# Kernel optimization log

Measured on AMD Instinct MI355X. Metric: run time of the kernel, lower is better.

The kernel has to match this reference:

```python
import jax, jax.numpy as jnp
import numpy as np

B = 1
E = 8388608                      # embedding size (dim 1)
NNZ = 131072                     # inhibition links
MIN_SPARSITY = 0.002
MAX_SPARSITY = 0.02
BOOST_PERCENT = 1e-8             # forward default boost_percent
MAX_ACTIVE = int(np.ceil(MAX_SPARSITY * E))    # 167773, torch uses .item() -> static
MIN_ACTIVE = int(np.floor(MIN_SPARSITY * E))   # 16777


def setup_inputs() -> dict:
    key = jax.random.key(0)
    k1, k3, k4, k5 = jax.random.split(key, 4)
    x = jax.random.normal(k1, (B, E, 1, 1), dtype=jnp.float32)
    boost_tensor = jnp.zeros((B, E, 1, 1), dtype=jnp.float32)   # initial boost state (zeros_like in module)
    inh_affector = jax.random.randint(k3, (NNZ,), 0, E, dtype=jnp.int32)
    inh_affectee = jax.random.randint(k4, (NNZ,), 0, E, dtype=jnp.int32)
    # inhibition values are negative (self-inhibition, affect_value=-0.01 scale)
    inh_values = -jax.random.uniform(k5, (NNZ,), dtype=jnp.float32) * 0.05
    return {"x": x, "boost_tensor": boost_tensor, "inh_values": inh_values,
            "inh_affector": inh_affector, "inh_affectee": inh_affectee}


def reference(x, boost_tensor, inh_values, inh_affector, inh_affectee):
    xf = x.reshape(B, E)
    bf = boost_tensor.reshape(B, E)

    # --- run_boosting: PercentClosenessBoosting (units far from max get boosted) ---
    boost_new = bf + (1.0 - xf / jnp.max(xf)) * jnp.float32(BOOST_PERCENT)
    boosted = jnp.maximum(xf, 0.0) + boost_new   # tensor_above + boost_tensor

    # --- apply_sparse_self_affector: tens[affectee] += tens[affector] * values ---
    # RHS gathered from the pre-update tensor, scatter-add onto affectee coords.
    inhibited = boosted.at[0, inh_affectee].add(boosted[0, inh_affector] * inh_values)

    # --- run_k_winners_positive: keep top max_active per row, binarize positives ---
    topv, topi = jax.lax.top_k(inhibited, MAX_ACTIVE)          # [B, K]
    rows = jnp.arange(B)[:, None]
    result = jnp.zeros((B, E), dtype=jnp.float32).at[rows, topi].set(
        (topv > 0).astype(jnp.float32))

    # --- choose_boosted_to_satisfy_minimum ---
    actually_active = jnp.sum(result)
    _, boost_idx = jax.lax.top_k(boost_new, MIN_ACTIVE)        # [B, MIN_ACTIVE]
    to_activate = jnp.ceil(jnp.float32(MIN_ACTIVE) - actually_active)
    need = actually_active < jnp.float32(MIN_ACTIVE)
    add = need & (jnp.arange(MIN_ACTIVE, dtype=jnp.float32) < to_activate)
    add = jnp.broadcast_to(add.astype(jnp.float32), (B, MIN_ACTIVE))
    out = result.at[rows, boost_idx].max(add)

    return out.reshape(B, E, 1, 1)
```

## Files before the change

kernel.cpp:

```cpp
#include <hip/hip_runtime.h>
#include <stdint.h>

#define E_SIZE   8388608
#define N4       (E_SIZE / 4)
#define NNZ_SZ   131072
#define K_ACT    167773
#define MIN_ACT  16777
#define CAP      262144
#define BCAP     2048
#define TINY_F   9.5367431640625e-7f
#define NBINS    16384
#define SHIFT1   18

__device__ __forceinline__ unsigned int f2A(float f) {
    unsigned int u = __float_as_uint(f);
    return (u & 0x80000000u) ? ~u : (u | 0x80000000u);
}
__device__ __forceinline__ unsigned int f2D(float f) { return ~f2A(f); }
__device__ __forceinline__ float A2f(unsigned int A) {
    unsigned int u = (A & 0x80000000u) ? (A & 0x7FFFFFFFu) : ~A;
    return __uint_as_float(u);
}
__device__ __forceinline__ float D2f(unsigned int D) { return A2f(~D); }

__device__ __forceinline__ float boostedf(float v, float b, float mx) {
    return fmaxf(v, 0.0f) + (b + (1.0f - v / mx) * 1e-8f);
}
__device__ __forceinline__ unsigned int binclamp14(float v) {
    return (v < TINY_F) ? (NBINS - 1u) : (f2D(v) >> SHIFT1);
}


__device__ void block_select(const unsigned int* counts, int nbins, unsigned int Krem,
                             unsigned int* res, unsigned int* scratch) {
    int t = threadIdx.x;
    int per = nbins >> 10; if (per == 0) per = 1;
    int nth = nbins / per;
    unsigned int part = 0;
    if (t < nth)
        for (int j = 0; j < per; j++) part += counts[t * per + j];
    scratch[t] = part;
    unsigned int ws = part;
    for (int off = 32; off; off >>= 1) ws += __shfl_down(ws, off, 64);
    if ((t & 63) == 0) scratch[1024 + (t >> 6)] = ws;
    __syncthreads();
    if (t == 0) {
        unsigned int cum = 0;
        int w = 0;
        for (; w < 15; w++) {
            unsigned int s = scratch[1024 + w];
            if (cum + s >= Krem) break;
            cum += s;
        }
        int tt = w * 64, te = tt + 63;
        for (; tt < te; tt++) {
            unsigned int s = scratch[tt];
            if (cum + s >= Krem) break;
            cum += s;
        }
        int b = tt * per, be = b + per - 1;
        for (; b < be; b++) {
            unsigned int s = counts[b];
            if (cum + s >= Krem) break;
            cum += s;
        }
        res[0] = (unsigned int)b;
        res[1] = Krem - cum;
    }
    __syncthreads();
}

__global__ void __launch_bounds__(256)
k_max(const float4* __restrict__ x, unsigned int* __restrict__ pmax,
      unsigned int* __restrict__ ctrl, unsigned int* __restrict__ hist) {
    int t = threadIdx.x, blk = blockIdx.x;
    if (blk == 0 && t < 64) ctrl[t] = 0u;
    if (t < 16) hist[blk * 16 + t] = 0u;
    int tid = blk * 256 + t;
    unsigned int m = 0u;
    for (int i = tid; i < N4; i += 1024 * 256) {
        float4 v = x[i];
        m = max(m, f2A(v.x)); m = max(m, f2A(v.y));
        m = max(m, f2A(v.z)); m = max(m, f2A(v.w));
    }
    for (int off = 32; off; off >>= 1)
        m = max(m, __shfl_down(m, off, 64));
    __shared__ unsigned int sm[4];
    if ((t & 63) == 0) sm[t >> 6] = m;
    __syncthreads();
    if (t == 0) pmax[blk] = max(max(sm[0], sm[1]), max(sm[2], sm[3]));
}

__device__ __forceinline__ float reduce_pmax(const unsigned int* __restrict__ pmax,
                                             unsigned int* smax) {
    int t = threadIdx.x;
    unsigned int m = pmax[t];
    for (int off = 32; off; off >>= 1)
        m = max(m, __shfl_down(m, off, 64));
    if ((t & 63) == 0) smax[t >> 6] = m;
    __syncthreads();
    if (t == 0) {
        unsigned int r = smax[0];
        for (int i = 1; i < 16; i++) r = max(r, smax[i]);
        smax[0] = r;
    }
    __syncthreads();
    return A2f(smax[0]);
}

__global__ void __launch_bounds__(1024)
k_boost_hist(const float4* __restrict__ x, const float4* __restrict__ bf,
             float4* __restrict__ out, const unsigned int* __restrict__ pmax,
             unsigned int* __restrict__ hist) {
    __shared__ unsigned int h[NBINS];
    __shared__ unsigned int smax[16];
    float mx = reduce_pmax(pmax, smax);
    int t = threadIdx.x;
    for (int i = t; i < NBINS; i += 1024) h[i] = 0u;
    __syncthreads();
    unsigned int tiny = 0;
    int gtid = blockIdx.x * 1024 + t;
    for (int i = gtid; i < N4; i += 512 * 1024) {
        float4 v = x[i], b = bf[i];
        float4 r;
        r.x = boostedf(v.x, b.x, mx);
        r.y = boostedf(v.y, b.y, mx);
        r.z = boostedf(v.z, b.z, mx);
        r.w = boostedf(v.w, b.w, mx);
        out[i] = r;
        #define HISTONE(c) { if ((c) < TINY_F) tiny++; \
            else atomicAdd(&h[f2D(c) >> SHIFT1], 1u); }
        HISTONE(r.x); HISTONE(r.y); HISTONE(r.z); HISTONE(r.w);
        #undef HISTONE
    }
    for (int off = 32; off; off >>= 1)
        tiny += __shfl_down(tiny, off, 64);
    if ((t & 63) == 0 && tiny) atomicAdd(&h[NBINS - 1], tiny);
    __syncthreads();
    for (int k = t; k < NBINS; k += 1024) {
        unsigned int c = h[k];
        if (c) atomicAdd(&hist[k], c);
    }
}

__global__ void __launch_bounds__(1024)
k_scatter(const float* __restrict__ x, const float* __restrict__ bf,
          const float* __restrict__ vals, const int* __restrict__ aff,
          const int* __restrict__ afe, float* __restrict__ inh,
          const unsigned int* __restrict__ pmax, unsigned int* __restrict__ hist) {
    __shared__ int shi[NBINS];
    __shared__ unsigned int smax[16];
    float mx = reduce_pmax(pmax, smax);
    int t = threadIdx.x;
    for (int i = t; i < NBINS; i += 1024) shi[i] = 0;
    __syncthreads();
    int i = blockIdx.x * 1024 + t;
    int a = aff[i], e = afe[i];
    float bo = boostedf(x[a], bf[a], mx);
    float contrib = bo * vals[i];
    float old = atomicAdd(&inh[e], contrib);
    float nw = old + contrib;
    unsigned int ob = binclamp14(old), nb = binclamp14(nw);
    if (ob != nb) {
        atomicAdd(&shi[nb], 1);
        atomicAdd(&shi[ob], -1);
    }
    __syncthreads();
    for (int k = t; k < NBINS; k += 1024) {
        int v = shi[k];
        if (v) atomicAdd((int*)&hist[k], v);
    }
}

__global__ void __launch_bounds__(1024)
k_markselect(float4* __restrict__ out, const unsigned int* __restrict__ hist,
             unsigned int* __restrict__ ctrl, unsigned int* __restrict__ gidx,
             unsigned int* __restrict__ gD) {
    __shared__ unsigned int scratch[1040];
    __shared__ unsigned int res[2];
    __shared__ unsigned int cidx[BCAP];
    __shared__ unsigned int cDs[BCAP];
    __shared__ unsigned int scnt, sbase;
    int t = threadIdx.x;
    if (t == 0) scnt = 0;
    block_select(hist, NBINS, (unsigned int)K_ACT, res, scratch);
    unsigned int b1 = res[0];
    if (blockIdx.x == 0 && t == 0) { ctrl[1] = res[0]; ctrl[2] = res[1]; }
    __syncthreads();
    int gtid = blockIdx.x * 1024 + t;
    for (int i = gtid; i < N4; i += 512 * 1024) {
        float4 f = out[i];
        float4 r;
        #define MARKONE(c, rr, comp) { \
            unsigned int bc = binclamp14(c); \
            if (bc < b1) rr = ((c) > 0.0f) ? 1.0f : 0.0f; \
            else { rr = 0.0f; if (bc == b1) { \
                unsigned int p = atomicAdd(&scnt, 1u); \
                if (p < BCAP) { cidx[p] = (unsigned int)i * 4u + comp; cDs[p] = f2D(c); } } } }
        MARKONE(f.x, r.x, 0u); MARKONE(f.y, r.y, 1u);
        MARKONE(f.z, r.z, 2u); MARKONE(f.w, r.w, 3u);
        #undef MARKONE
        out[i] = r;
    }
    __syncthreads();
    if (t == 0) {
        unsigned int m = min(scnt, (unsigned int)BCAP);
        scnt = m;
        sbase = atomicAdd(&ctrl[7], m);
    }
    __syncthreads();
    unsigned int m = scnt, base = sbase;
    for (unsigned int i = t; i < m; i += 1024) {
        unsigned int g = base + i;
        if (g < CAP) { gidx[g] = cidx[i]; gD[g] = cDs[i]; }
    }
}

__global__ void __launch_bounds__(1024)
k_select(float* __restrict__ out, const unsigned int* __restrict__ ctrl,
         const unsigned int* __restrict__ gidx, const unsigned int* __restrict__ gD) {
    __shared__ unsigned int h512[512];
    __shared__ unsigned int scratch[1040];
    __shared__ unsigned int res[2];
    __shared__ unsigned int ties[128];
    __shared__ unsigned int tcnt;
    int t = threadIdx.x;
    unsigned int nc = min(ctrl[7], (unsigned int)CAP);
    unsigned int Krem = ctrl[2];
    unsigned int b1 = ctrl[1];

    if (t < 512) h512[t] = 0u;
    if (t == 0) tcnt = 0u;
    __syncthreads();
    for (unsigned int i = t; i < nc; i += 1024)
        atomicAdd(&h512[(gD[i] >> 9) & 511u], 1u);
    __syncthreads();
    block_select(h512, 512, Krem, res, scratch);
    unsigned int b2 = res[0], Krem2 = res[1];

    if (t < 512) h512[t] = 0u;
    __syncthreads();
    for (unsigned int i = t; i < nc; i += 1024) {
        unsigned int D = gD[i];
        if (((D >> 9) & 511u) == b2) atomicAdd(&h512[D & 511u], 1u);
    }
    __syncthreads();
    block_select(h512, 512, Krem2, res, scratch);
    unsigned int b3 = res[0], need = res[1];
    unsigned int T = (b1 << SHIFT1) | (b2 << 9) | b3;

    for (unsigned int i = t; i < nc; i += 1024) {
        if (gD[i] == T) {
            unsigned int p = atomicAdd(&tcnt, 1u);
            if (p < 128) ties[p] = gidx[i];
        }
    }
    __syncthreads();
    unsigned int M = min(tcnt, 128u);
    float val = (D2f(T) > 0.0f) ? 1.0f : 0.0f;
    for (unsigned int i = t; i < M; i += 1024) {
        unsigned int idx = ties[i];
        unsigned int rank = 0;
        for (unsigned int j = 0; j < M; j++) rank += (ties[j] < idx) ? 1u : 0u;
        if (rank < need) out[idx] = val;
    }
    for (unsigned int i = t; i < nc; i += 1024) {
        unsigned int D = gD[i];
        if (D < T) out[gidx[i]] = (D2f(D) > 0.0f) ? 1.0f : 0.0f;
    }
}

extern "C" void kernel_launch(void* const* d_in, const int* in_sizes, int n_in,
                              void* d_out, int out_size, void* d_ws, size_t ws_size,
                              hipStream_t stream) {
    const float* x    = (const float*)d_in[0];
    const float* bf   = (const float*)d_in[1];
    const float* vals = (const float*)d_in[2];
    const int*   aff  = (const int*)d_in[3];
    const int*   afe  = (const int*)d_in[4];
    float* out = (float*)d_out;

    unsigned int* ctrl = (unsigned int*)d_ws;
    unsigned int* pmax = (unsigned int*)((char*)d_ws + 4096);
    unsigned int* hist = (unsigned int*)((char*)d_ws + 16384);
    unsigned int* gidx = (unsigned int*)((char*)d_ws + 16384 + (size_t)NBINS * 4);
    unsigned int* gD   = (unsigned int*)((char*)d_ws + 16384 + (size_t)NBINS * 4 + (size_t)CAP * 4);

    k_max<<<1024, 256, 0, stream>>>((const float4*)x, pmax, ctrl, hist);
    k_boost_hist<<<512, 1024, 0, stream>>>((const float4*)x, (const float4*)bf,
                                           (float4*)out, pmax, hist);
    k_scatter<<<NNZ_SZ / 1024, 1024, 0, stream>>>(x, bf, vals, aff, afe, out, pmax, hist);
    k_markselect<<<512, 1024, 0, stream>>>((float4*)out, hist, ctrl, gidx, gD);
    k_select<<<1, 1024, 0, stream>>>(out, ctrl, gidx, gD);
}
```

Before: 190.4 us.

## Fuse max, boost-histogram, scatter and selection into two kernels with grid barriers

```diff
diff --git a/kernel.cpp b/kernel.cpp
--- a/kernel.cpp
+++ b/kernel.cpp
@@ -11,6 +11,11 @@
 #define TINY_F   9.5367431640625e-7f
 #define NBINS    16384
 #define SHIFT1   18
+#define G1       256
+#define G2       512
+
+#define AL(p)  __hip_atomic_load((p), __ATOMIC_RELAXED, __HIP_MEMORY_SCOPE_AGENT)
+#define ALA(p) __hip_atomic_load((p), __ATOMIC_ACQUIRE, __HIP_MEMORY_SCOPE_AGENT)
 
 __device__ __forceinline__ unsigned int f2A(float f) {
     unsigned int u = __float_as_uint(f);
@@ -30,6 +35,14 @@
     return (v < TINY_F) ? (NBINS - 1u) : (f2D(v) >> SHIFT1);
 }
 
+
+__device__ __forceinline__ void grid_spin_barrier(unsigned int* ctr, unsigned int n) {
+    if (threadIdx.x == 0) {
+        __hip_atomic_fetch_add(ctr, 1u, __ATOMIC_ACQ_REL, __HIP_MEMORY_SCOPE_AGENT);
+        while (ALA(ctr) < n) __builtin_amdgcn_s_sleep(1);
+    }
+    __syncthreads();
+}
 
 __device__ void block_select(const unsigned int* counts, int nbins, unsigned int Krem,
                              unsigned int* res, unsigned int* scratch) {
@@ -70,178 +83,207 @@
     __syncthreads();
 }
 
-__global__ void __launch_bounds__(256)
-k_max(const float4* __restrict__ x, unsigned int* __restrict__ pmax,
-      unsigned int* __restrict__ ctrl, unsigned int* __restrict__ hist) {
+__device__ void block_select_g(unsigned int* counts, int nbins, unsigned int Krem,
+                               unsigned int* res, unsigned int* scratch) {
+    int t = threadIdx.x;
+    int per = nbins >> 10;
+    unsigned int part = 0;
+    for (int j = 0; j < per; j++) part += AL(&counts[t * per + j]);
+    scratch[t] = part;
+    unsigned int ws = part;
+    for (int off = 32; off; off >>= 1) ws += __shfl_down(ws, off, 64);
+    if ((t & 63) == 0) scratch[1024 + (t >> 6)] = ws;
+    __syncthreads();
+    if (t == 0) {
+        unsigned int cum = 0;
+        int w = 0;
+        for (; w < 15; w++) {
+            unsigned int s = scratch[1024 + w];
+            if (cum + s >= Krem) break;
+            cum += s;
+        }
+        int tt = w * 64, te = tt + 63;
+        for (; tt < te; tt++) {
+            unsigned int s = scratch[tt];
+            if (cum + s >= Krem) break;
+            cum += s;
+        }
+        int b = tt * per, be = b + per - 1;
+        for (; b < be; b++) {
+            unsigned int s = AL(&counts[b]);
+            if (cum + s >= Krem) break;
+            cum += s;
+        }
+        res[0] = (unsigned int)b;
+        res[1] = Krem - cum;
+    }
+    __syncthreads();
+}
+
+__global__ void __launch_bounds__(1024)
+k_fused1(const float4* __restrict__ x4, const float4* __restrict__ bf4,
+         const float* __restrict__ x, const float* __restrict__ bf,
+         const float* __restrict__ vals, const int* __restrict__ aff,
+         const int* __restrict__ afe, float* __restrict__ out,
+         unsigned int* __restrict__ ctrl, unsigned int* __restrict__ hist) {
+    __shared__ unsigned int h[NBINS];
+    __shared__ unsigned int smax[20];
+    float4* out4 = (float4*)out;
     int t = threadIdx.x, blk = blockIdx.x;
-    if (blk == 0 && t < 64) ctrl[t] = 0u;
-    if (t < 16) hist[blk * 16 + t] = 0u;
-    int tid = blk * 256 + t;
-    unsigned int m = 0u;
-    for (int i = tid; i < N4; i += 1024 * 256) {
-        float4 v = x[i];
-        m = max(m, f2A(v.x)); m = max(m, f2A(v.y));
-        m = max(m, f2A(v.z)); m = max(m, f2A(v.w));
-    }
-    for (int off = 32; off; off >>= 1)
-        m = max(m, __shfl_down(m, off, 64));
-    __shared__ unsigned int sm[4];
-    if ((t & 63) == 0) sm[t >> 6] = m;
-    __syncthreads();
-    if (t == 0) pmax[blk] = max(max(sm[0], sm[1]), max(sm[2], sm[3]));
-}
-
-__device__ __forceinline__ float reduce_pmax(const unsigned int* __restrict__ pmax,
-                                             unsigned int* smax) {
-    int t = threadIdx.x;
-    unsigned int m = pmax[t];
-    for (int off = 32; off; off >>= 1)
-        m = max(m, __shfl_down(m, off, 64));
-    if ((t & 63) == 0) smax[t >> 6] = m;
-    __syncthreads();
-    if (t == 0) {
-        unsigned int r = smax[0];
-        for (int i = 1; i < 16; i++) r = max(r, smax[i]);
-        smax[0] = r;
-    }
-    __syncthreads();
-    return A2f(smax[0]);
-}
-
-__global__ void __launch_bounds__(1024)
-k_boost_hist(const float4* __restrict__ x, const float4* __restrict__ bf,
-             float4* __restrict__ out, const unsigned int* __restrict__ pmax,
-             unsigned int* __restrict__ hist) {
-    __shared__ unsigned int h[NBINS];
-    __shared__ unsigned int smax[16];
-    float mx = reduce_pmax(pmax, smax);
-    int t = threadIdx.x;
+    int gtid = blk * 1024 + t;
+
+    {
+        unsigned int m = 0u;
+        for (int i = gtid; i < N4; i += G1 * 1024) {
+            float4 v = x4[i];
+            m = max(m, f2A(v.x)); m = max(m, f2A(v.y));
+            m = max(m, f2A(v.z)); m = max(m, f2A(v.w));
+        }
+        for (int off = 32; off; off >>= 1)
+            m = max(m, __shfl_down(m, off, 64));
+        if ((t & 63) == 0) smax[t >> 6] = m;
+        __syncthreads();
+        if (t == 0) {
+            unsigned int r = smax[0];
+            for (int i = 1; i < 16; i++) r = max(r, smax[i]);
+            atomicMax(&ctrl[0], r);
+        }
+    }
+    grid_spin_barrier(&ctrl[8], G1);
+    if (t == 0) smax[16] = AL(&ctrl[0]);
     for (int i = t; i < NBINS; i += 1024) h[i] = 0u;
     __syncthreads();
-    unsigned int tiny = 0;
-    int gtid = blockIdx.x * 1024 + t;
-    for (int i = gtid; i < N4; i += 512 * 1024) {
-        float4 v = x[i], b = bf[i];
-        float4 r;
-        r.x = boostedf(v.x, b.x, mx);
-        r.y = boostedf(v.y, b.y, mx);
-        r.z = boostedf(v.z, b.z, mx);
-        r.w = boostedf(v.w, b.w, mx);
-        out[i] = r;
-        #define HISTONE(c) { if ((c) < TINY_F) tiny++; \
-            else atomicAdd(&h[f2D(c) >> SHIFT1], 1u); }
-        HISTONE(r.x); HISTONE(r.y); HISTONE(r.z); HISTONE(r.w);
-        #undef HISTONE
-    }
-    for (int off = 32; off; off >>= 1)
-        tiny += __shfl_down(tiny, off, 64);
-    if ((t & 63) == 0 && tiny) atomicAdd(&h[NBINS - 1], tiny);
+    float mx = A2f(smax[16]);
+
+    {
+        unsigned int tiny = 0;
+        for (int i = gtid; i < N4; i += G1 * 1024) {
+            float4 v = x4[i], b = bf4[i];
+            float4 r;
+            r.x = boostedf(v.x, b.x, mx);
+            r.y = boostedf(v.y, b.y, mx);
+            r.z = boostedf(v.z, b.z, mx);
+            r.w = boostedf(v.w, b.w, mx);
+            out4[i] = r;
+            #define HISTONE(c) { if ((c) < TINY_F) tiny++; \
+                else atomicAdd(&h[f2D(c) >> SHIFT1], 1u); }
+            HISTONE(r.x); HISTONE(r.y); HISTONE(r.z); HISTONE(r.w);
+            #undef HISTONE
+        }
+        for (int off = 32; off; off >>= 1)
+            tiny += __shfl_down(tiny, off, 64);
+        if ((t & 63) == 0 && tiny) atomicAdd(&h[NBINS - 1], tiny);
+    }
     __syncthreads();
     for (int k = t; k < NBINS; k += 1024) {
         unsigned int c = h[k];
         if (c) atomicAdd(&hist[k], c);
     }
+    __threadfence();
+    grid_spin_barrier(&ctrl[9], G1);
+
+    {
+        int* shi = (int*)h;
+        for (int i = t; i < NBINS; i += 1024) shi[i] = 0;
+        __syncthreads();
+        if (gtid < NNZ_SZ) {
+            int a = aff[gtid], e = afe[gtid];
+            float bo = boostedf(x[a], bf[a], mx);
+            float contrib = bo * vals[gtid];
+            float old = atomicAdd(&out[e], contrib);
+            float nw = old + contrib;
+            unsigned int ob = binclamp14(old), nb = binclamp14(nw);
+            if (ob != nb) {
+                atomicAdd(&shi[nb], 1);
+                atomicAdd(&shi[ob], -1);
+            }
+        }
+        __syncthreads();
+        for (int k = t; k < NBINS; k += 1024) {
+            int v = shi[k];
+            if (v) atomicAdd((int*)&hist[k], v);
+        }
+    }
+    __threadfence();
+
+    if (t == 0)
+        smax[17] = __hip_atomic_fetch_add(&ctrl[10], 1u, __ATOMIC_ACQ_REL,
+                                          __HIP_MEMORY_SCOPE_AGENT);
+    __syncthreads();
+    if (smax[17] == G1 - 1) {
+        __shared__ unsigned int res[2];
+        block_select_g(hist, NBINS, (unsigned int)K_ACT, res, h);
+        if (t == 0) { ctrl[1] = res[0]; ctrl[2] = res[1]; }
+    }
 }
 
 __global__ void __launch_bounds__(1024)
-k_scatter(const float* __restrict__ x, const float* __restrict__ bf,
-          const float* __restrict__ vals, const int* __restrict__ aff,
-          const int* __restrict__ afe, float* __restrict__ inh,
-          const unsigned int* __restrict__ pmax, unsigned int* __restrict__ hist) {
-    __shared__ int shi[NBINS];
-    __shared__ unsigned int smax[16];
-    float mx = reduce_pmax(pmax, smax);
-    int t = threadIdx.x;
-    for (int i = t; i < NBINS; i += 1024) shi[i] = 0;
-    __syncthreads();
-    int i = blockIdx.x * 1024 + t;
-    int a = aff[i], e = afe[i];
-    float bo = boostedf(x[a], bf[a], mx);
-    float contrib = bo * vals[i];
-    float old = atomicAdd(&inh[e], contrib);
-    float nw = old + contrib;
-    unsigned int ob = binclamp14(old), nb = binclamp14(nw);
-    if (ob != nb) {
-        atomicAdd(&shi[nb], 1);
-        atomicAdd(&shi[ob], -1);
-    }
-    __syncthreads();
-    for (int k = t; k < NBINS; k += 1024) {
-        int v = shi[k];
-        if (v) atomicAdd((int*)&hist[k], v);
-    }
-}
-
-__global__ void __launch_bounds__(1024)
-k_markselect(float4* __restrict__ out, const unsigned int* __restrict__ hist,
-             unsigned int* __restrict__ ctrl, unsigned int* __restrict__ gidx,
-             unsigned int* __restrict__ gD) {
-    __shared__ unsigned int scratch[1040];
-    __shared__ unsigned int res[2];
+k_fused2(float4* __restrict__ out4, float* __restrict__ out,
+         unsigned int* __restrict__ ctrl, unsigned int* __restrict__ gidx,
+         unsigned int* __restrict__ gD) {
     __shared__ unsigned int cidx[BCAP];
     __shared__ unsigned int cDs[BCAP];
-    __shared__ unsigned int scnt, sbase;
-    int t = threadIdx.x;
-    if (t == 0) scnt = 0;
-    block_select(hist, NBINS, (unsigned int)K_ACT, res, scratch);
-    unsigned int b1 = res[0];
-    if (blockIdx.x == 0 && t == 0) { ctrl[1] = res[0]; ctrl[2] = res[1]; }
-    __syncthreads();
-    int gtid = blockIdx.x * 1024 + t;
-    for (int i = gtid; i < N4; i += 512 * 1024) {
-        float4 f = out[i];
+    __shared__ unsigned int scratch[1040];
+    __shared__ unsigned int sst[8];
+    __shared__ unsigned int ties[128];
+    int t = threadIdx.x, blk = blockIdx.x;
+    if (t == 0) sst[0] = 0;
+    __syncthreads();
+    unsigned int b1 = ctrl[1];
+    unsigned int Krem = ctrl[2];
+    int gtid = blk * 1024 + t;
+
+    for (int i = gtid; i < N4; i += G2 * 1024) {
+        float4 f = out4[i];
         float4 r;
         #define MARKONE(c, rr, comp) { \
             unsigned int bc = binclamp14(c); \
             if (bc < b1) rr = ((c) > 0.0f) ? 1.0f : 0.0f; \
             else { rr = 0.0f; if (bc == b1) { \
-                unsigned int p = atomicAdd(&scnt, 1u); \
+                unsigned int p = atomicAdd(&sst[0], 1u); \
                 if (p < BCAP) { cidx[p] = (unsigned int)i * 4u + comp; cDs[p] = f2D(c); } } } }
         MARKONE(f.x, r.x, 0u); MARKONE(f.y, r.y, 1u);
         MARKONE(f.z, r.z, 2u); MARKONE(f.w, r.w, 3u);
         #undef MARKONE
-        out[i] = r;
+        out4[i] = r;
     }
     __syncthreads();
     if (t == 0) {
-        unsigned int m = min(scnt, (unsigned int)BCAP);
-        scnt = m;
-        sbase = atomicAdd(&ctrl[7], m);
-    }
-    __syncthreads();
-    unsigned int m = scnt, base = sbase;
-    for (unsigned int i = t; i < m; i += 1024) {
-        unsigned int g = base + i;
-        if (g < CAP) { gidx[g] = cidx[i]; gD[g] = cDs[i]; }
-    }
-}
-
-__global__ void __launch_bounds__(1024)
-k_select(float* __restrict__ out, const unsigned int* __restrict__ ctrl,
-         const unsigned int* __restrict__ gidx, const unsigned int* __restrict__ gD) {
-    __shared__ unsigned int h512[512];
-    __shared__ unsigned int scratch[1040];
+        unsigned int m = min(sst[0], (unsigned int)BCAP);
+        sst[0] = m;
+        sst[1] = atomicAdd(&ctrl[7], m);
+    }
+    __syncthreads();
+    {
+        unsigned int m = sst[0], base = sst[1];
+        for (unsigned int i = t; i < m; i += 1024) {
+            unsigned int g = base + i;
+            if (g < CAP) { gidx[g] = cidx[i]; gD[g] = cDs[i]; }
+        }
+    }
+    __threadfence();
+    if (t == 0)
+        sst[2] = __hip_atomic_fetch_add(&ctrl[11], 1u, __ATOMIC_ACQ_REL,
+                                        __HIP_MEMORY_SCOPE_AGENT);
+    __syncthreads();
+    if (sst[2] != G2 - 1) return;
+
+    unsigned int nc = min(AL(&ctrl[7]), (unsigned int)CAP);
+    unsigned int* h512 = cidx;
+    if (t < 512) h512[t] = 0u;
+    if (t == 0) sst[3] = 0u;
+    __syncthreads();
+    for (unsigned int i = t; i < nc; i += 1024)
+        atomicAdd(&h512[(AL(&gD[i]) >> 9) & 511u], 1u);
+    __syncthreads();
     __shared__ unsigned int res[2];
-    __shared__ unsigned int ties[128];
-    __shared__ unsigned int tcnt;
-    int t = threadIdx.x;
-    unsigned int nc = min(ctrl[7], (unsigned int)CAP);
-    unsigned int Krem = ctrl[2];
-    unsigned int b1 = ctrl[1];
-
-    if (t < 512) h512[t] = 0u;
-    if (t == 0) tcnt = 0u;
-    __syncthreads();
-    for (unsigned int i = t; i < nc; i += 1024)
-        atomicAdd(&h512[(gD[i] >> 9) & 511u], 1u);
-    __syncthreads();
     block_select(h512, 512, Krem, res, scratch);
     unsigned int b2 = res[0], Krem2 = res[1];
 
     if (t < 512) h512[t] = 0u;
     __syncthreads();
     for (unsigned int i = t; i < nc; i += 1024) {
-        unsigned int D = gD[i];
+        unsigned int D = AL(&gD[i]);
         if (((D >> 9) & 511u) == b2) atomicAdd(&h512[D & 511u], 1u);
     }
     __syncthreads();
@@ -250,13 +292,13 @@
     unsigned int T = (b1 << SHIFT1) | (b2 << 9) | b3;
 
     for (unsigned int i = t; i < nc; i += 1024) {
-        if (gD[i] == T) {
-            unsigned int p = atomicAdd(&tcnt, 1u);
-            if (p < 128) ties[p] = gidx[i];
-        }
-    }
-    __syncthreads();
-    unsigned int M = min(tcnt, 128u);
+        if (AL(&gD[i]) == T) {
+            unsigned int p = atomicAdd(&sst[3], 1u);
+            if (p < 128) ties[p] = AL(&gidx[i]);
+        }
+    }
+    __syncthreads();
+    unsigned int M = min(sst[3], 128u);
     float val = (D2f(T) > 0.0f) ? 1.0f : 0.0f;
     for (unsigned int i = t; i < M; i += 1024) {
         unsigned int idx = ties[i];
@@ -265,8 +307,8 @@
         if (rank < need) out[idx] = val;
     }
     for (unsigned int i = t; i < nc; i += 1024) {
-        unsigned int D = gD[i];
-        if (D < T) out[gidx[i]] = (D2f(D) > 0.0f) ? 1.0f : 0.0f;
+        unsigned int D = AL(&gD[i]);
+        if (D < T) out[AL(&gidx[i])] = (D2f(D) > 0.0f) ? 1.0f : 0.0f;
     }
 }
 
@@ -281,15 +323,13 @@
     float* out = (float*)d_out;
 
     unsigned int* ctrl = (unsigned int*)d_ws;
-    unsigned int* pmax = (unsigned int*)((char*)d_ws + 4096);
-    unsigned int* hist = (unsigned int*)((char*)d_ws + 16384);
-    unsigned int* gidx = (unsigned int*)((char*)d_ws + 16384 + (size_t)NBINS * 4);
-    unsigned int* gD   = (unsigned int*)((char*)d_ws + 16384 + (size_t)NBINS * 4 + (size_t)CAP * 4);
-
-    k_max<<<1024, 256, 0, stream>>>((const float4*)x, pmax, ctrl, hist);
-    k_boost_hist<<<512, 1024, 0, stream>>>((const float4*)x, (const float4*)bf,
-                                           (float4*)out, pmax, hist);
-    k_scatter<<<NNZ_SZ / 1024, 1024, 0, stream>>>(x, bf, vals, aff, afe, out, pmax, hist);
-    k_markselect<<<512, 1024, 0, stream>>>((float4*)out, hist, ctrl, gidx, gD);
-    k_select<<<1, 1024, 0, stream>>>(out, ctrl, gidx, gD);
-}
+    unsigned int* hist = (unsigned int*)((char*)d_ws + 1024);
+    unsigned int* gidx = (unsigned int*)((char*)d_ws + 131072);
+    unsigned int* gD   = (unsigned int*)((char*)d_ws + 131072 + (size_t)CAP * 4);
+
+    hipMemsetAsync(d_ws, 0, 1024 + NBINS * 4, stream);
+
+    k_fused1<<<G1, 1024, 0, stream>>>((const float4*)x, (const float4*)bf,
+                                      x, bf, vals, aff, afe, out, ctrl, hist);
+    k_fused2<<<G2, 1024, 0, stream>>>((float4*)out, out, ctrl, gidx, gD);
+}
```

After: 514.4 us. +170.2%, slower.
